# Kernel optimization log

Hardware: AMD Instinct MI355X
Metric: run time of the kernel (lower is better)

The kernel has to match this reference:

```python
import jax, jax.numpy as jnp
import numpy as np

B, D, H, O = 8192, 1024, 4096, 1024
E, S = 8, 2  # routed experts, shared experts


def setup_inputs() -> dict:
    key = jax.random.key(0)
    ks = jax.random.split(key, 12)
    sd = lambda n: 1.0 / np.sqrt(n)
    return {
        "x": jax.random.normal(ks[0], (B, D), jnp.float32),
        "W1": jax.random.normal(ks[1], (E, D, H), jnp.float32) * sd(D),
        "b1": jnp.zeros((E, H), jnp.float32),
        "W2": jax.random.normal(ks[2], (E, H, O), jnp.float32) * sd(H),
        "b2": jnp.zeros((E, O), jnp.float32),
        "Ws1": jax.random.normal(ks[3], (S, D, H), jnp.float32) * sd(D),
        "bs1": jnp.zeros((S, H), jnp.float32),
        "Ws2": jax.random.normal(ks[4], (S, H, O), jnp.float32) * sd(H),
        "bs2": jnp.zeros((S, O), jnp.float32),
        "Wg": jax.random.normal(ks[5], (D, E + S), jnp.float32) * sd(D),
        "bg": jnp.zeros((E + S,), jnp.float32),
        "k": 2,
    }


def _expert_mlp(x, W1, b1, W2, b2):
    # x: [B,D], W1: [n,D,H] -> [B,n,O]; dropout is identity in eval mode
    h = jax.nn.relu(jnp.einsum("bd,ndh->bnh", x, W1) + b1[None])
    return jnp.einsum("bnh,nho->bno", h, W2) + b2[None]


def reference(x, W1, b1, W2, b2, Ws1, bs1, Ws2, bs2, Wg, bg, k):
    gate_scores = jax.nn.softmax(x @ Wg + bg, axis=-1)        # [B, S+E]
    shared_gate = gate_scores[:, :S]                          # [B, S]
    expert_gate = gate_scores[:, S:]                          # [B, E]

    expert_outputs = _expert_mlp(x, W1, b1, W2, b2)           # [B, E, O]
    shared_outputs = _expert_mlp(x, Ws1, bs1, Ws2, bs2)       # [B, S, O]
    shared_output = jnp.einsum("bs,bso->bo", shared_gate, shared_outputs)

    # sparse top-k combine (vectorized equivalent of the per-sample loop)
    topk_score, topk_idx = jax.lax.top_k(expert_gate, k)      # [B, k]
    gathered = jnp.take_along_axis(expert_outputs, topk_idx[:, :, None], axis=1)  # [B,k,O]
    output = jnp.einsum("bk,bko->bo", topk_score, gathered) + shared_output
    return output
```

## Files before the change

kernel.cpp:

```cpp
#include <hip/hip_runtime.h>
#include <stdint.h>

#define Bn 8192
#define Dn 1024
#define Hn 4096
#define On 1024
#define En 8
#define Sn 2

typedef __attribute__((ext_vector_type(8))) short short8;
typedef __attribute__((ext_vector_type(4))) float f32x4;
typedef __attribute__((ext_vector_type(16))) float f32x16;

__device__ __forceinline__ unsigned short f2bf(float f) {
  unsigned int u = __float_as_uint(f);
  u += 0x7fff + ((u >> 16) & 1);
  return (unsigned short)(u >> 16);
}

__device__ __forceinline__ void gload16(const void* g, void* l) {
  __builtin_amdgcn_global_load_lds(
      (const __attribute__((address_space(1))) unsigned int*)g,
      (__attribute__((address_space(3))) unsigned int*)l, 16, 0, 0);
}

__global__ __launch_bounds__(256) void gate_k(
    const float* __restrict__ x, const float* __restrict__ Wg,
    const float* __restrict__ bg, unsigned short* __restrict__ xb,
    float* __restrict__ rw, int* __restrict__ ri) {
  {
    size_t base = (size_t)blockIdx.x * 1024;
    const float4* xi = (const float4*)x + base;
    ushort4* xo = (ushort4*)xb + base;
#pragma unroll
    for (int k2 = 0; k2 < 4; k2++) {
      float4 v = xi[k2 * 256 + threadIdx.x];
      ushort4 o;
      o.x = f2bf(v.x); o.y = f2bf(v.y); o.z = f2bf(v.z); o.w = f2bf(v.w);
      xo[k2 * 256 + threadIdx.x] = o;
    }
  }
  __shared__ __align__(16) float wgs[Dn * 10];
  for (int i = threadIdx.x; i < 2560; i += 256)
    ((float4*)wgs)[i] = ((const float4*)Wg)[i];
  __syncthreads();
  int lane = threadIdx.x & 63, wave = threadIdx.x >> 6;
  int r = blockIdx.x * 4 + wave;
  const float* xr = x + (size_t)r * Dn;
  float p[10];
#pragma unroll
  for (int j = 0; j < 10; j++) p[j] = 0.f;
  for (int d = lane; d < Dn; d += 64) {
    float xv = xr[d];
#pragma unroll
    for (int j = 0; j < 10; j++) p[j] += xv * wgs[d * 10 + j];
  }
#pragma unroll
  for (int off = 32; off; off >>= 1)
#pragma unroll
    for (int j = 0; j < 10; j++) p[j] += __shfl_xor(p[j], off);
  float mx = -1e30f;
#pragma unroll
  for (int j = 0; j < 10; j++) { p[j] += bg[j]; mx = fmaxf(mx, p[j]); }
  float s = 0.f;
#pragma unroll
  for (int j = 0; j < 10; j++) { p[j] = expf(p[j] - mx); s += p[j]; }
  float inv = 1.f / s;
  int i0 = 2, i1 = 2; float v0 = -1e30f, v1 = -1e30f;
#pragma unroll
  for (int j = 2; j < 10; j++) {
    float v = p[j];
    if (v > v0) { v1 = v0; i1 = i0; v0 = v; i0 = j; }
    else if (v > v1) { v1 = v; i1 = j; }
  }
  if (lane == 0) {
    rw[r * 4 + 0] = v0 * inv;
    rw[r * 4 + 1] = v1 * inv;
    rw[r * 4 + 2] = p[0] * inv;
    rw[r * 4 + 3] = p[1] * inv;
    ri[r * 2 + 0] = i0 - 2;
    ri[r * 2 + 1] = i1 - 2;
  }
}

__global__ __launch_bounds__(256) void count_k(const int* __restrict__ ri,
                                               int* __restrict__ cnt) {
  int c[8];
#pragma unroll
  for (int j = 0; j < 8; j++) c[j] = 0;
  int base = blockIdx.x * 1024;
  for (int i = threadIdx.x; i < 1024; i += 256) {
    int e = ri[base + i];
#pragma unroll
    for (int j = 0; j < 8; j++) c[j] += (e == j) ? 1 : 0;
  }
#pragma unroll
  for (int j = 0; j < 8; j++)
#pragma unroll
    for (int off = 32; off; off >>= 1) c[j] += __shfl_xor(c[j], off);
  __shared__ int sc[4][8];
  int wv = threadIdx.x >> 6, lane = threadIdx.x & 63;
  if (lane == 0)
#pragma unroll
    for (int j = 0; j < 8; j++) sc[wv][j] = c[j];
  __syncthreads();
  if (threadIdx.x < 8)
    atomicAdd(&cnt[threadIdx.x], sc[0][threadIdx.x] + sc[1][threadIdx.x] +
                                 sc[2][threadIdx.x] + sc[3][threadIdx.x]);
}

__global__ __launch_bounds__(256) void tcvt_all(
    const float* __restrict__ W1, const float* __restrict__ W2,
    const float* __restrict__ Ws1, const float* __restrict__ Ws2,
    unsigned short* __restrict__ w1t, unsigned short* __restrict__ w2t,
    unsigned short* __restrict__ ws1t, unsigned short* __restrict__ ws2t) {
  __shared__ float t[128][65];
  int bid = blockIdx.x;
  int u = bid >> 9, r = bid & 511;
  const float* in; unsigned short* out; int Kd, Nd;
  if (u < 8)       { Kd = Dn; Nd = Hn; in = W1  + (size_t)u * Dn * Hn;        out = w1t  + (size_t)u * Dn * Hn; }
  else if (u < 16) { Kd = Hn; Nd = On; in = W2  + (size_t)(u - 8) * Hn * On;  out = w2t  + (size_t)(u - 8) * Hn * On; }
  else if (u < 18) { Kd = Dn; Nd = Hn; in = Ws1 + (size_t)(u - 16) * Dn * Hn; out = ws1t + (size_t)(u - 16) * Dn * Hn; }
  else             { Kd = Hn; Nd = On; in = Ws2 + (size_t)(u - 18) * Hn * On; out = ws2t + (size_t)(u - 18) * Hn * On; }
  int by, bx;
  if (Kd == Dn) { by = (r & 7) * 128;  bx = (r >> 3) * 64; }
  else          { by = (r & 31) * 128; bx = (r >> 5) * 64; }
  int tid = threadIdx.x;
#pragma unroll
  for (int q = 0; q < 8; q++) {
    int idx = q * 256 + tid;
    int k = idx >> 4, f4 = (idx & 15) * 4;
    float4 v = *(const float4*)&in[(size_t)(by + k) * Nd + bx + f4];
    t[k][f4] = v.x; t[k][f4 + 1] = v.y; t[k][f4 + 2] = v.z; t[k][f4 + 3] = v.w;
  }
  __syncthreads();
  int KC = Kd >> 3;
#pragma unroll
  for (int p = 0; p < 4; p++) {
    int idx = p * 256 + tid;
    int nl = idx & 63, kgi = idx >> 6;
    int kg = kgi * 8;
    int ng = bx + nl;
    short8 v;
#pragma unroll
    for (int j = 0; j < 8; j++) v[j] = (short)f2bf(t[kg + j][nl]);
    size_t o = ((((size_t)(ng >> 8) * KC + (by >> 3) + kgi) * 256 + (ng & 255)) << 3);
    *(short8*)&out[o] = v;
  }
}

__global__ __launch_bounds__(256) void build_k(
    const float* __restrict__ rw, const int* __restrict__ ri,
    const int* __restrict__ cnt, int* __restrict__ cnt2,
    int* __restrict__ slot_row, float* __restrict__ slot_w,
    int* __restrict__ slot_dst) {
  __shared__ int lcnt[8], lbase[8];
  int tid = threadIdx.x;
  if (tid < 8) lcnt[tid] = 0;
  __syncthreads();
  int r = blockIdx.x * 256 + tid;
  int e0 = ri[r * 2 + 0], e1 = ri[r * 2 + 1];
  int rk0 = atomicAdd(&lcnt[e0], 1);
  int rk1 = atomicAdd(&lcnt[e1], 1);
  __syncthreads();
  if (tid < 8) lbase[tid] = atomicAdd(&cnt2[tid], lcnt[tid]);
  __syncthreads();
  int off0 = 0, off1 = 0;
#pragma unroll
  for (int i = 0; i < 8; i++) {
    int ci = cnt[i];
    off0 += (i < e0) ? ci : 0;
    off1 += (i < e1) ? ci : 0;
  }
  int s0 = off0 + lbase[e0] + rk0;
  int s1 = off1 + lbase[e1] + rk1;
  slot_row[s0] = r; slot_w[s0] = rw[r * 4 + 0]; slot_dst[s0] = r * 4 + 0;
  slot_row[s1] = r; slot_w[s1] = rw[r * 4 + 1]; slot_dst[s1] = r * 4 + 1;
#pragma unroll
  for (int s = 0; s < 2; s++) {
    int slot = 16384 + s * Bn + r;
    slot_row[slot] = r;
    slot_w[slot] = rw[r * 4 + 2 + s];
    slot_dst[slot] = r * 4 + 2 + s;
  }
}


__global__ __launch_bounds__(512, 4) void gemm1_u(
    const unsigned short* __restrict__ xb,
    const unsigned short* __restrict__ w1c, const unsigned short* __restrict__ ws1c,
    const float* __restrict__ b1, const float* __restrict__ bs1,
    const int* __restrict__ cnt, const int* __restrict__ slotRow,
    unsigned short* __restrict__ h, int ubase, int hsh) {
  int total = gridDim.x;
  int gid = blockIdx.x;
  int swz = (gid & 7) * (total >> 3) + (gid >> 3);
  int u = ubase + (swz >> 10);
  int rem = swz & 1023;
  int mt = rem & 63;
  int nt = rem >> 6;

  int M, off, hoff;
  const unsigned short* Bte; const float* be;
  if (u < 8) {
    M = cnt[u]; off = 0;
    for (int i = 0; i < u; i++) off += cnt[i];
    hoff = off;
    Bte = w1c + (size_t)u * Hn * Dn; be = b1 + (size_t)u * Hn;
  } else {
    int s = u - 8;
    M = Bn; off = 16384 + s * Bn; hoff = hsh + s * Bn;
    Bte = ws1c + (size_t)s * Hn * Dn; be = bs1 + (size_t)s * Hn;
  }
  int mbase = mt * 128;
  if (mbase >= M) return;
  int n0 = nt * 256;

  __shared__ __align__(16) unsigned short shb[36864];

  int tid = threadIdx.x;
  int lane = tid & 63, wv = tid >> 6;
  int wm = wv >> 2, wn = wv & 3;
  int l31 = lane & 31, l5 = lane >> 5;
  int rswA = (l31 >> 1) & 3;

  int scol = (((tid & 3) ^ ((tid >> 3) & 3)) * 8);
  int mi = mbase + (tid >> 2);
  if (mi > M - 1) mi = M - 1;
  int grow = slotRow[off + mi];
  const unsigned short* agp = xb + (size_t)grow * Dn + scol;
  const unsigned short* Bnt = Bte + (size_t)nt * 262144;
  const unsigned short* bgp0 = Bnt + (((size_t)(tid >> 8) * 256 + (tid & 255)) << 3);
  const unsigned short* bgp1 = bgp0 + 4096;

  f32x16 acc[2][2];
#pragma unroll
  for (int i = 0; i < 2; i++)
#pragma unroll
    for (int j = 0; j < 2; j++)
#pragma unroll
      for (int q = 0; q < 16; q++) acc[i][j][q] = 0.f;

  auto STAGE = [&](int slot, int tt) {
    int so = slot * 12288;
    gload16(agp + tt * 32, &shb[so + wv * 512]);
    gload16(bgp0 + tt * 8192, &shb[so + 4096 + wv * 512]);
    gload16(bgp1 + tt * 8192, &shb[so + 8192 + wv * 512]);
  };
  auto COMPUTE = [&](int slot) {
    int so = slot * 12288;
#pragma unroll
    for (int kk = 0; kk < 2; kk++) {
      int cA = (((kk * 2 + l5) ^ rswA) * 8);
      short8 a0 = *(const short8*)&shb[so + (wm * 64 + l31) * 32 + cA];
      short8 a1 = *(const short8*)&shb[so + (wm * 64 + 32 + l31) * 32 + cA];
      int cB = (kk * 2 + l5) * 256;
      short8 b0 = *(const short8*)&shb[so + 4096 + (cB + wn * 64 + l31) * 8];
      short8 b1 = *(const short8*)&shb[so + 4096 + (cB + wn * 64 + 32 + l31) * 8];
      acc[0][0] = __builtin_amdgcn_mfma_f32_32x32x16_bf16(a0, b0, acc[0][0], 0, 0, 0);
      acc[0][1] = __builtin_amdgcn_mfma_f32_32x32x16_bf16(a0, b1, acc[0][1], 0, 0, 0);
      acc[1][0] = __builtin_amdgcn_mfma_f32_32x32x16_bf16(a1, b0, acc[1][0], 0, 0, 0);
      acc[1][1] = __builtin_amdgcn_mfma_f32_32x32x16_bf16(a1, b1, acc[1][1], 0, 0, 0);
    }
  };

  const int NT = Dn >> 5;
  int sA = 0, sB = 1, sC = 2;
  STAGE(0, 0);
  STAGE(1, 1);
  for (int t = 0; t < NT; ++t) {
    int tn = (t + 2 < NT) ? (t + 2) : (NT - 1);
    STAGE(sC, tn);
    asm volatile("s_waitcnt vmcnt(6)" ::: "memory");
    asm volatile("s_barrier" ::: "memory");
    COMPUTE(sA);
    asm volatile("s_barrier" ::: "memory");
    int tmp = sA; sA = sB; sB = sC; sC = tmp;
  }

  float bev[2];
#pragma unroll
  for (int g = 0; g < 2; g++) bev[g] = be[n0 + wn * 64 + g * 32 + l31];
#pragma unroll
  for (int i = 0; i < 2; i++) {
#pragma unroll
    for (int reg = 0; reg < 16; reg++) {
      int rr = (reg & 3) + 8 * (reg >> 2) + 4 * l5;
      int m = mbase + wm * 64 + i * 32 + rr;
      if (m < M) {
        size_t hrow = (size_t)(hoff + m) * Hn;
#pragma unroll
        for (int g = 0; g < 2; g++) {
          int n = n0 + wn * 64 + g * 32 + l31;
          float v = acc[i][g][reg] + bev[g];
          h[hrow + n] = f2bf(fmaxf(v, 0.f));
        }
      }
    }
  }
}

__global__ __launch_bounds__(512, 4) void gemm2_u(
    const unsigned short* __restrict__ hin,
    const unsigned short* __restrict__ w2c, const unsigned short* __restrict__ ws2c,
    const float* __restrict__ b2, const float* __restrict__ bs2,
    const int* __restrict__ cnt, const float* __restrict__ slotW,
    const int* __restrict__ slotDst, float* __restrict__ outp, int ubase, int hsh) {
  int total = gridDim.x;
  int gid = blockIdx.x;
  int swz = (gid & 7) * (total >> 3) + (gid >> 3);
  int u = ubase + (swz >> 8);
  int rem = swz & 255;
  int mt = rem & 63;
  int nt = rem >> 6;

  int M, off, hoff;
  const unsigned short* Bte; const float* be;
  if (u < 8) {
    M = cnt[u]; off = 0;
    for (int i = 0; i < u; i++) off += cnt[i];
    hoff = off;
    Bte = w2c + (size_t)u * On * Hn; be = b2 + (size_t)u * On;
  } else {
    int s = u - 8;
    M = Bn; off = 16384 + s * Bn; hoff = hsh + s * Bn;
    Bte = ws2c + (size_t)s * On * Hn; be = bs2 + (size_t)s * On;
  }
  int mbase = mt * 128;
  if (mbase >= M) return;
  int n0 = nt * 256;

  __shared__ __align__(16) unsigned short shb[36864];

  int tid = threadIdx.x;
  int lane = tid & 63, wv = tid >> 6;
  int wm = wv >> 2, wn = wv & 3;
  int l31 = lane & 31, l5 = lane >> 5;
  int rswA = (l31 >> 1) & 3;

  int scol = (((tid & 3) ^ ((tid >> 3) & 3)) * 8);
  int mi = mbase + (tid >> 2);
  if (mi > M - 1) mi = M - 1;
  const unsigned short* agp = hin + (size_t)(hoff + mi) * Hn + scol;
  const unsigned short* Bnt = Bte + (size_t)nt * 1048576;
  const unsigned short* bgp0 = Bnt + (((size_t)(tid >> 8) * 256 + (tid & 255)) << 3);
  const unsigned short* bgp1 = bgp0 + 4096;

  f32x16 acc[2][2];
#pragma unroll
  for (int i = 0; i < 2; i++)
#pragma unroll
    for (int j = 0; j < 2; j++)
#pragma unroll
      for (int q = 0; q < 16; q++) acc[i][j][q] = 0.f;

  auto STAGE = [&](int slot, int tt) {
    int so = slot * 12288;
    gload16(agp + tt * 32, &shb[so + wv * 512]);
    gload16(bgp0 + tt * 8192, &shb[so + 4096 + wv * 512]);
    gload16(bgp1 + tt * 8192, &shb[so + 8192 + wv * 512]);
  };
  auto COMPUTE = [&](int slot) {
    int so = slot * 12288;
#pragma unroll
    for (int kk = 0; kk < 2; kk++) {
      int cA = (((kk * 2 + l5) ^ rswA) * 8);
      short8 a0 = *(const short8*)&shb[so + (wm * 64 + l31) * 32 + cA];
      short8 a1 = *(const short8*)&shb[so + (wm * 64 + 32 + l31) * 32 + cA];
      int cB = (kk * 2 + l5) * 256;
      short8 b0 = *(const short8*)&shb[so + 4096 + (cB + wn * 64 + l31) * 8];
      short8 b1 = *(const short8*)&shb[so + 4096 + (cB + wn * 64 + 32 + l31) * 8];
      acc[0][0] = __builtin_amdgcn_mfma_f32_32x32x16_bf16(a0, b0, acc[0][0], 0, 0, 0);
      acc[0][1] = __builtin_amdgcn_mfma_f32_32x32x16_bf16(a0, b1, acc[0][1], 0, 0, 0);
      acc[1][0] = __builtin_amdgcn_mfma_f32_32x32x16_bf16(a1, b0, acc[1][0], 0, 0, 0);
      acc[1][1] = __builtin_amdgcn_mfma_f32_32x32x16_bf16(a1, b1, acc[1][1], 0, 0, 0);
    }
  };

  const int NT = Hn >> 5;
  int sA = 0, sB = 1, sC = 2;
  STAGE(0, 0);
  STAGE(1, 1);
  for (int t = 0; t < NT; ++t) {
    int tn = (t + 2 < NT) ? (t + 2) : (NT - 1);
    STAGE(sC, tn);
    asm volatile("s_waitcnt vmcnt(6)" ::: "memory");
    asm volatile("s_barrier" ::: "memory");
    COMPUTE(sA);
    asm volatile("s_barrier" ::: "memory");
    int tmp = sA; sA = sB; sB = sC; sC = tmp;
  }

  float bev[2];
#pragma unroll
  for (int g = 0; g < 2; g++) bev[g] = be[n0 + wn * 64 + g * 32 + l31];
#pragma unroll
  for (int i = 0; i < 2; i++) {
#pragma unroll
    for (int reg = 0; reg < 16; reg++) {
      int rr = (reg & 3) + 8 * (reg >> 2) + 4 * l5;
      int m = mbase + wm * 64 + i * 32 + rr;
      if (m < M) {
        float wgt = slotW[off + m];
        size_t orow = (size_t)(slotDst[off + m] >> 2) * On;
#pragma unroll
        for (int g = 0; g < 2; g++) {
          int n = n0 + wn * 64 + g * 32 + l31;
          atomicAdd(&outp[orow + n], wgt * (acc[i][g][reg] + bev[g]));
        }
      }
    }
  }
}

extern "C" void kernel_launch(void* const* d_in, const int* in_sizes, int n_in,
                              void* d_out, int out_size, void* d_ws, size_t ws_size,
                              hipStream_t stream) {
  const float* x   = (const float*)d_in[0];
  const float* W1  = (const float*)d_in[1];
  const float* b1  = (const float*)d_in[2];
  const float* W2  = (const float*)d_in[3];
  const float* b2  = (const float*)d_in[4];
  const float* Ws1 = (const float*)d_in[5];
  const float* bs1 = (const float*)d_in[6];
  const float* Ws2 = (const float*)d_in[7];
  const float* bs2 = (const float*)d_in[8];
  const float* Wg  = (const float*)d_in[9];
  const float* bg  = (const float*)d_in[10];
  float* out = (float*)d_out;

  char* w = (char*)d_ws;
  size_t p = 0;
  auto alloc = [&](size_t n) { char* r = w + p; p = (p + n + 255) & ~(size_t)255; return r; };
  unsigned short* xb   = (unsigned short*)alloc((size_t)Bn * Dn * 2);
  unsigned short* w1t  = (unsigned short*)alloc((size_t)En * Hn * Dn * 2);
  unsigned short* w2t  = (unsigned short*)alloc((size_t)En * On * Hn * 2);
  unsigned short* ws1t = (unsigned short*)alloc((size_t)Sn * Hn * Dn * 2);
  unsigned short* ws2t = (unsigned short*)alloc((size_t)Sn * On * Hn * 2);
  unsigned short* hbuf = (unsigned short*)alloc((size_t)16384 * Hn * 2);
  float* rw            = (float*)alloc((size_t)Bn * 4 * 4);
  int* ri              = (int*)alloc((size_t)Bn * 2 * 4);
  int* ctrl            = (int*)alloc(256);
  int* slot_row        = (int*)alloc((size_t)32768 * 4);
  float* slot_w        = (float*)alloc((size_t)32768 * 4);
  int* slot_dst        = (int*)alloc((size_t)32768 * 4);
  if (p > ws_size) return;

  int* cnt  = ctrl;
  int* cnt2 = ctrl + 8;

  hipMemsetAsync(ctrl, 0, 64, stream);
  hipMemsetAsync(out, 0, (size_t)Bn * On * sizeof(float), stream);
  gate_k<<<2048, 256, 0, stream>>>(x, Wg, bg, xb, rw, ri);
  tcvt_all<<<10240, 256, 0, stream>>>(W1, W2, Ws1, Ws2, w1t, w2t, ws1t, ws2t);
  count_k<<<16, 256, 0, stream>>>(ri, cnt);
  build_k<<<32, 256, 0, stream>>>(rw, ri, cnt, cnt2, slot_row, slot_w, slot_dst);

  gemm1_u<<<8 * 1024, 512, 0, stream>>>(xb, w1t, ws1t, b1, bs1, cnt, slot_row,
                                        hbuf, 0, 0);
  gemm2_u<<<8 * 256, 512, 0, stream>>>(hbuf, w2t, ws2t, b2, bs2, cnt, slot_w,
                                       slot_dst, out, 0, 0);
  gemm1_u<<<2 * 1024, 512, 0, stream>>>(xb, w1t, ws1t, b1, bs1, cnt, slot_row,
                                        hbuf, 8, 0);
  gemm2_u<<<2 * 256, 512, 0, stream>>>(hbuf, w2t, ws2t, b2, bs2, cnt, slot_w,
                                       slot_dst, out, 8, 0);
}
```

Before: 873.7 us.

## Use double-buffered LDS pipeline and replace atomic combine with per-slot buffer reduction

Both GEMM kernels drop from a triple-buffered to a double-buffered LDS pipeline, cutting shared memory per block so more blocks fit per CU (launch bounds raised to 6). The GEMM2 epilogue now writes weighted outputs to a per-(row, slot) buffer Y instead of doing atomicAdd into the output. A new final kernel sums the four slots per row, which also removes the output memset. This trades atomic contention for an extra 128MB write and read pass, and shortens prefetch depth, which may expose load latency.

```diff
diff --git a/kernel.cpp b/kernel.cpp
--- a/kernel.cpp
+++ b/kernel.cpp
@@ -186,7 +186,7 @@
 }
 
 
-__global__ __launch_bounds__(512, 4) void gemm1_u(
+__global__ __launch_bounds__(512, 6) void gemm1_u(
     const unsigned short* __restrict__ xb,
     const unsigned short* __restrict__ w1c, const unsigned short* __restrict__ ws1c,
     const float* __restrict__ b1, const float* __restrict__ bs1,
@@ -216,7 +216,7 @@
   if (mbase >= M) return;
   int n0 = nt * 256;
 
-  __shared__ __align__(16) unsigned short shb[36864];
+  __shared__ __align__(16) unsigned short shb[24576];
 
   int tid = threadIdx.x;
   int lane = tid & 63, wv = tid >> 6;
@@ -265,17 +265,16 @@
   };
 
   const int NT = Dn >> 5;
-  int sA = 0, sB = 1, sC = 2;
   STAGE(0, 0);
-  STAGE(1, 1);
+  int cur = 0;
   for (int t = 0; t < NT; ++t) {
-    int tn = (t + 2 < NT) ? (t + 2) : (NT - 1);
-    STAGE(sC, tn);
-    asm volatile("s_waitcnt vmcnt(6)" ::: "memory");
+    int tn = (t + 1 < NT) ? (t + 1) : (NT - 1);
+    STAGE(cur ^ 1, tn);
+    asm volatile("s_waitcnt vmcnt(3)" ::: "memory");
     asm volatile("s_barrier" ::: "memory");
-    COMPUTE(sA);
+    COMPUTE(cur);
     asm volatile("s_barrier" ::: "memory");
-    int tmp = sA; sA = sB; sB = sC; sC = tmp;
+    cur ^= 1;
   }
 
   float bev[2];
@@ -300,12 +299,12 @@
   }
 }
 
-__global__ __launch_bounds__(512, 4) void gemm2_u(
+__global__ __launch_bounds__(512, 6) void gemm2_u(
     const unsigned short* __restrict__ hin,
     const unsigned short* __restrict__ w2c, const unsigned short* __restrict__ ws2c,
     const float* __restrict__ b2, const float* __restrict__ bs2,
     const int* __restrict__ cnt, const float* __restrict__ slotW,
-    const int* __restrict__ slotDst, float* __restrict__ outp, int ubase, int hsh) {
+    const int* __restrict__ slotDst, float* __restrict__ Y, int ubase, int hsh) {
   int total = gridDim.x;
   int gid = blockIdx.x;
   int swz = (gid & 7) * (total >> 3) + (gid >> 3);
@@ -330,7 +329,7 @@
   if (mbase >= M) return;
   int n0 = nt * 256;
 
-  __shared__ __align__(16) unsigned short shb[36864];
+  __shared__ __align__(16) unsigned short shb[24576];
 
   int tid = threadIdx.x;
   int lane = tid & 63, wv = tid >> 6;
@@ -378,17 +377,16 @@
   };
 
   const int NT = Hn >> 5;
-  int sA = 0, sB = 1, sC = 2;
   STAGE(0, 0);
-  STAGE(1, 1);
+  int cur = 0;
   for (int t = 0; t < NT; ++t) {
-    int tn = (t + 2 < NT) ? (t + 2) : (NT - 1);
-    STAGE(sC, tn);
-    asm volatile("s_waitcnt vmcnt(6)" ::: "memory");
+    int tn = (t + 1 < NT) ? (t + 1) : (NT - 1);
+    STAGE(cur ^ 1, tn);
+    asm volatile("s_waitcnt vmcnt(3)" ::: "memory");
     asm volatile("s_barrier" ::: "memory");
-    COMPUTE(sA);
+    COMPUTE(cur);
     asm volatile("s_barrier" ::: "memory");
-    int tmp = sA; sA = sB; sB = sC; sC = tmp;
+    cur ^= 1;
   }
 
   float bev[2];
@@ -402,15 +400,32 @@
       int m = mbase + wm * 64 + i * 32 + rr;
       if (m < M) {
         float wgt = slotW[off + m];
-        size_t orow = (size_t)(slotDst[off + m] >> 2) * On;
+        size_t yrow = (size_t)slotDst[off + m] * On;
 #pragma unroll
         for (int g = 0; g < 2; g++) {
           int n = n0 + wn * 64 + g * 32 + l31;
-          atomicAdd(&outp[orow + n], wgt * (acc[i][g][reg] + bev[g]));
+          Y[yrow + n] = wgt * (acc[i][g][reg] + bev[g]);
         }
       }
     }
   }
+}
+
+__global__ void final_k(const float* __restrict__ Y, float* __restrict__ out) {
+  int i = blockIdx.x * 256 + threadIdx.x;
+  int b = i >> 8;
+  int c = i & 255;
+  const float4* y = (const float4*)Y;
+  float4 a0 = y[((size_t)b * 4 + 0) * 256 + c];
+  float4 a1 = y[((size_t)b * 4 + 1) * 256 + c];
+  float4 a2 = y[((size_t)b * 4 + 2) * 256 + c];
+  float4 a3 = y[((size_t)b * 4 + 3) * 256 + c];
+  float4 o;
+  o.x = a0.x + a1.x + a2.x + a3.x;
+  o.y = a0.y + a1.y + a2.y + a3.y;
+  o.z = a0.z + a1.z + a2.z + a3.z;
+  o.w = a0.w + a1.w + a2.w + a3.w;
+  ((float4*)out)[i] = o;
 }
 
 extern "C" void kernel_launch(void* const* d_in, const int* in_sizes, int n_in,
@@ -438,6 +453,7 @@
   unsigned short* ws1t = (unsigned short*)alloc((size_t)Sn * Hn * Dn * 2);
   unsigned short* ws2t = (unsigned short*)alloc((size_t)Sn * On * Hn * 2);
   unsigned short* hbuf = (unsigned short*)alloc((size_t)16384 * Hn * 2);
+  float* Y             = (float*)alloc((size_t)Bn * 4 * On * 4);
   float* rw            = (float*)alloc((size_t)Bn * 4 * 4);
   int* ri              = (int*)alloc((size_t)Bn * 2 * 4);
   int* ctrl            = (int*)alloc(256);
@@ -450,7 +466,6 @@
   int* cnt2 = ctrl + 8;
 
   hipMemsetAsync(ctrl, 0, 64, stream);
-  hipMemsetAsync(out, 0, (size_t)Bn * On * sizeof(float), stream);
   gate_k<<<2048, 256, 0, stream>>>(x, Wg, bg, xb, rw, ri);
   tcvt_all<<<10240, 256, 0, stream>>>(W1, W2, Ws1, Ws2, w1t, w2t, ws1t, ws2t);
   count_k<<<16, 256, 0, stream>>>(ri, cnt);
@@ -459,9 +474,10 @@
   gemm1_u<<<8 * 1024, 512, 0, stream>>>(xb, w1t, ws1t, b1, bs1, cnt, slot_row,
                                         hbuf, 0, 0);
   gemm2_u<<<8 * 256, 512, 0, stream>>>(hbuf, w2t, ws2t, b2, bs2, cnt, slot_w,
-                                       slot_dst, out, 0, 0);
+                                       slot_dst, Y, 0, 0);
   gemm1_u<<<2 * 1024, 512, 0, stream>>>(xb, w1t, ws1t, b1, bs1, cnt, slot_row,
                                         hbuf, 8, 0);
   gemm2_u<<<2 * 256, 512, 0, stream>>>(hbuf, w2t, ws2t, b2, bs2, cnt, slot_w,
-                                       slot_dst, out, 8, 0);
-}
+                                       slot_dst, Y, 8, 0);
+  final_k<<<8192, 256, 0, stream>>>(Y, out);
+}
```

Result: slower. 1.458 ms (+66.9%).

## Replace atomic output accumulation with staged buffer and fused shared-expert combine

Applied to the files above, without the earlier changes.

Routed-expert GEMM2 now writes weighted results non-atomically into a per-(row,k) staging buffer Y instead of atomically adding into the output. A new shared-expert GEMM2 kernel computes both shared experts per tile, applies gate weights, adds the two routed contributions from Y, and writes the final output directly, which removes the output memset and all float atomics. It adds a 64MB intermediate buffer write/read and a serial two-phase K loop per block with smaller N tiles.

```diff
diff --git a/kernel.cpp b/kernel.cpp
--- a/kernel.cpp
+++ b/kernel.cpp
@@ -174,14 +174,14 @@
   }
   int s0 = off0 + lbase[e0] + rk0;
   int s1 = off1 + lbase[e1] + rk1;
-  slot_row[s0] = r; slot_w[s0] = rw[r * 4 + 0]; slot_dst[s0] = r * 4 + 0;
-  slot_row[s1] = r; slot_w[s1] = rw[r * 4 + 1]; slot_dst[s1] = r * 4 + 1;
+  slot_row[s0] = r; slot_w[s0] = rw[r * 4 + 0]; slot_dst[s0] = r * 2 + 0;
+  slot_row[s1] = r; slot_w[s1] = rw[r * 4 + 1]; slot_dst[s1] = r * 2 + 1;
 #pragma unroll
   for (int s = 0; s < 2; s++) {
     int slot = 16384 + s * Bn + r;
     slot_row[slot] = r;
     slot_w[slot] = rw[r * 4 + 2 + s];
-    slot_dst[slot] = r * 4 + 2 + s;
+    slot_dst[slot] = 0;
   }
 }
 
@@ -302,30 +302,24 @@
 
 __global__ __launch_bounds__(512, 4) void gemm2_u(
     const unsigned short* __restrict__ hin,
-    const unsigned short* __restrict__ w2c, const unsigned short* __restrict__ ws2c,
-    const float* __restrict__ b2, const float* __restrict__ bs2,
+    const unsigned short* __restrict__ w2c,
+    const float* __restrict__ b2,
     const int* __restrict__ cnt, const float* __restrict__ slotW,
-    const int* __restrict__ slotDst, float* __restrict__ outp, int ubase, int hsh) {
+    const int* __restrict__ slotDst, float* __restrict__ Y) {
   int total = gridDim.x;
   int gid = blockIdx.x;
   int swz = (gid & 7) * (total >> 3) + (gid >> 3);
-  int u = ubase + (swz >> 8);
+  int u = swz >> 8;
   int rem = swz & 255;
   int mt = rem & 63;
   int nt = rem >> 6;
 
-  int M, off, hoff;
-  const unsigned short* Bte; const float* be;
-  if (u < 8) {
-    M = cnt[u]; off = 0;
-    for (int i = 0; i < u; i++) off += cnt[i];
-    hoff = off;
-    Bte = w2c + (size_t)u * On * Hn; be = b2 + (size_t)u * On;
-  } else {
-    int s = u - 8;
-    M = Bn; off = 16384 + s * Bn; hoff = hsh + s * Bn;
-    Bte = ws2c + (size_t)s * On * Hn; be = bs2 + (size_t)s * On;
-  }
+  int M = cnt[u], off = 0;
+  for (int i = 0; i < u; i++) off += cnt[i];
+  int hoff = off;
+  const unsigned short* Bte = w2c + (size_t)u * On * Hn;
+  const float* be = b2 + (size_t)u * On;
+
   int mbase = mt * 128;
   if (mbase >= M) return;
   int n0 = nt * 256;
@@ -402,13 +396,112 @@
       int m = mbase + wm * 64 + i * 32 + rr;
       if (m < M) {
         float wgt = slotW[off + m];
-        size_t orow = (size_t)(slotDst[off + m] >> 2) * On;
+        size_t yrow = (size_t)slotDst[off + m] * On;
 #pragma unroll
         for (int g = 0; g < 2; g++) {
           int n = n0 + wn * 64 + g * 32 + l31;
-          atomicAdd(&outp[orow + n], wgt * (acc[i][g][reg] + bev[g]));
+          Y[yrow + n] = wgt * (acc[i][g][reg] + bev[g]);
         }
       }
+    }
+  }
+}
+
+__global__ __launch_bounds__(512, 4) void gemm2s_m(
+    const unsigned short* __restrict__ hin,
+    const unsigned short* __restrict__ ws2c,
+    const float* __restrict__ bs2, const float* __restrict__ rw,
+    const float* __restrict__ Y, float* __restrict__ outp) {
+  int total = gridDim.x;
+  int gid = blockIdx.x;
+  int swz = (gid & 7) * (total >> 3) + (gid >> 3);
+  int mt = swz & 63;
+  int nt = swz >> 6;
+  int mbase = mt * 128;
+  int n0 = nt * 128;
+
+  __shared__ __align__(16) unsigned short shb[24576];
+
+  int tid = threadIdx.x;
+  int lane = tid & 63, wv = tid >> 6;
+  int wm = wv >> 2, wn = wv & 3;
+  int l31 = lane & 31, l5 = lane >> 5;
+  int rswA = (l31 >> 1) & 3;
+
+  int scol = (((tid & 3) ^ ((tid >> 3) & 3)) * 8);
+  const unsigned short* agp0 = hin + (size_t)(mbase + (tid >> 2)) * Hn + scol;
+  const unsigned short* agp1 = agp0 + (size_t)8192 * Hn;
+  size_t bcol = (((size_t)(tid >> 7) * 256 + (nt & 1) * 128 + (tid & 127)) << 3);
+  const unsigned short* bgp0 = ws2c + (size_t)(nt >> 1) * 1048576 + bcol;
+  const unsigned short* bgp1 = bgp0 + (size_t)Hn * On;
+
+  f32x16 acc0[2], acc1[2];
+#pragma unroll
+  for (int i = 0; i < 2; i++)
+#pragma unroll
+    for (int q = 0; q < 16; q++) { acc0[i][q] = 0.f; acc1[i][q] = 0.f; }
+
+  auto STAGE = [&](int slot, int tt, const unsigned short* ag, const unsigned short* bg) {
+    int so = slot * 8192;
+    gload16(ag + tt * 32, &shb[so + wv * 512]);
+    gload16(bg + (size_t)tt * 8192, &shb[so + 4096 + wv * 512]);
+  };
+  auto COMPUTE = [&](int slot, f32x16 (&ac)[2]) {
+    int so = slot * 8192;
+#pragma unroll
+    for (int kk = 0; kk < 2; kk++) {
+      int cA = (((kk * 2 + l5) ^ rswA) * 8);
+      short8 a0 = *(const short8*)&shb[so + (wm * 64 + l31) * 32 + cA];
+      short8 a1 = *(const short8*)&shb[so + (wm * 64 + 32 + l31) * 32 + cA];
+      int cB = (kk * 2 + l5) * 128;
+      short8 b0 = *(const short8*)&shb[so + 4096 + (cB + wn * 32 + l31) * 8];
+      ac[0] = __builtin_amdgcn_mfma_f32_32x32x16_bf16(a0, b0, ac[0], 0, 0, 0);
+      ac[1] = __builtin_amdgcn_mfma_f32_32x32x16_bf16(a1, b0, ac[1], 0, 0, 0);
+    }
+  };
+
+  {
+    int sA = 0, sB = 1, sC = 2;
+    STAGE(0, 0, agp0, bgp0);
+    STAGE(1, 1, agp0, bgp0);
+    for (int t = 0; t < 128; ++t) {
+      int tn = (t + 2 < 128) ? (t + 2) : 127;
+      STAGE(sC, tn, agp0, bgp0);
+      asm volatile("s_waitcnt vmcnt(4)" ::: "memory");
+      asm volatile("s_barrier" ::: "memory");
+      COMPUTE(sA, acc0);
+      asm volatile("s_barrier" ::: "memory");
+      int tmp = sA; sA = sB; sB = sC; sC = tmp;
+    }
+  }
+  {
+    int sA = 0, sB = 1, sC = 2;
+    STAGE(0, 0, agp1, bgp1);
+    STAGE(1, 1, agp1, bgp1);
+    for (int t = 0; t < 128; ++t) {
+      int tn = (t + 2 < 128) ? (t + 2) : 127;
+      STAGE(sC, tn, agp1, bgp1);
+      asm volatile("s_waitcnt vmcnt(4)" ::: "memory");
+      asm volatile("s_barrier" ::: "memory");
+      COMPUTE(sA, acc1);
+      asm volatile("s_barrier" ::: "memory");
+      int tmp = sA; sA = sB; sB = sC; sC = tmp;
+    }
+  }
+
+  int n = n0 + wn * 32 + l31;
+  float be0 = bs2[n];
+  float be1 = bs2[On + n];
+#pragma unroll
+  for (int i = 0; i < 2; i++) {
+#pragma unroll
+    for (int reg = 0; reg < 16; reg++) {
+      int rr = (reg & 3) + 8 * (reg >> 2) + 4 * l5;
+      int m = mbase + wm * 64 + i * 32 + rr;
+      float w0 = rw[m * 4 + 2], w1 = rw[m * 4 + 3];
+      float v = w0 * (acc0[i][reg] + be0) + w1 * (acc1[i][reg] + be1)
+              + Y[((size_t)m * 2 + 0) * On + n] + Y[((size_t)m * 2 + 1) * On + n];
+      outp[(size_t)m * On + n] = v;
     }
   }
 }
@@ -438,6 +531,7 @@
   unsigned short* ws1t = (unsigned short*)alloc((size_t)Sn * Hn * Dn * 2);
   unsigned short* ws2t = (unsigned short*)alloc((size_t)Sn * On * Hn * 2);
   unsigned short* hbuf = (unsigned short*)alloc((size_t)16384 * Hn * 2);
+  float* Y             = (float*)alloc((size_t)Bn * 2 * On * 4);
   float* rw            = (float*)alloc((size_t)Bn * 4 * 4);
   int* ri              = (int*)alloc((size_t)Bn * 2 * 4);
   int* ctrl            = (int*)alloc(256);
@@ -450,7 +544,6 @@
   int* cnt2 = ctrl + 8;
 
   hipMemsetAsync(ctrl, 0, 64, stream);
-  hipMemsetAsync(out, 0, (size_t)Bn * On * sizeof(float), stream);
   gate_k<<<2048, 256, 0, stream>>>(x, Wg, bg, xb, rw, ri);
   tcvt_all<<<10240, 256, 0, stream>>>(W1, W2, Ws1, Ws2, w1t, w2t, ws1t, ws2t);
   count_k<<<16, 256, 0, stream>>>(ri, cnt);
@@ -458,10 +551,8 @@
 
   gemm1_u<<<8 * 1024, 512, 0, stream>>>(xb, w1t, ws1t, b1, bs1, cnt, slot_row,
                                         hbuf, 0, 0);
-  gemm2_u<<<8 * 256, 512, 0, stream>>>(hbuf, w2t, ws2t, b2, bs2, cnt, slot_w,
-                                       slot_dst, out, 0, 0);
+  gemm2_u<<<8 * 256, 512, 0, stream>>>(hbuf, w2t, b2, cnt, slot_w, slot_dst, Y);
   gemm1_u<<<2 * 1024, 512, 0, stream>>>(xb, w1t, ws1t, b1, bs1, cnt, slot_row,
                                         hbuf, 8, 0);
-  gemm2_u<<<2 * 256, 512, 0, stream>>>(hbuf, w2t, ws2t, b2, bs2, cnt, slot_w,
-                                       slot_dst, out, 8, 0);
-}
+  gemm2s_m<<<512, 512, 0, stream>>>(hbuf, ws2t, bs2, rw, Y, out);
+}
```

After: 859.6 us. About the same (-1.6%).

## Replace atomic output accumulation with per-slot buffer and final reduction kernel

Applied to the files above, without the earlier changes.

gemm2 now writes each weighted expert contribution into a dedicated slot of a [B,4,O] buffer instead of issuing float atomicAdds into the output, and a new final_k kernel sums the four slots per row. This also removes the output memset. The bf16 conversion of x is folded into the gate kernel's existing row loop, and the weight transpose kernel now reads global memory directly instead of staging through an LDS tile. The goal is to cut atomic contention and memset traffic, at the cost of an extra 128MB write plus read. The uncoalesced strided reads in the transpose kernel may cost more than the LDS staging they replace.

```diff
diff --git a/kernel.cpp b/kernel.cpp
--- a/kernel.cpp
+++ b/kernel.cpp
@@ -28,18 +28,6 @@
     const float* __restrict__ x, const float* __restrict__ Wg,
     const float* __restrict__ bg, unsigned short* __restrict__ xb,
     float* __restrict__ rw, int* __restrict__ ri) {
-  {
-    size_t base = (size_t)blockIdx.x * 1024;
-    const float4* xi = (const float4*)x + base;
-    ushort4* xo = (ushort4*)xb + base;
-#pragma unroll
-    for (int k2 = 0; k2 < 4; k2++) {
-      float4 v = xi[k2 * 256 + threadIdx.x];
-      ushort4 o;
-      o.x = f2bf(v.x); o.y = f2bf(v.y); o.z = f2bf(v.z); o.w = f2bf(v.w);
-      xo[k2 * 256 + threadIdx.x] = o;
-    }
-  }
   __shared__ __align__(16) float wgs[Dn * 10];
   for (int i = threadIdx.x; i < 2560; i += 256)
     ((float4*)wgs)[i] = ((const float4*)Wg)[i];
@@ -47,11 +35,13 @@
   int lane = threadIdx.x & 63, wave = threadIdx.x >> 6;
   int r = blockIdx.x * 4 + wave;
   const float* xr = x + (size_t)r * Dn;
+  unsigned short* xbr = xb + (size_t)r * Dn;
   float p[10];
 #pragma unroll
   for (int j = 0; j < 10; j++) p[j] = 0.f;
   for (int d = lane; d < Dn; d += 64) {
     float xv = xr[d];
+    xbr[d] = f2bf(xv);
 #pragma unroll
     for (int j = 0; j < 10; j++) p[j] += xv * wgs[d * 10 + j];
   }
@@ -114,7 +104,6 @@
     const float* __restrict__ Ws1, const float* __restrict__ Ws2,
     unsigned short* __restrict__ w1t, unsigned short* __restrict__ w2t,
     unsigned short* __restrict__ ws1t, unsigned short* __restrict__ ws2t) {
-  __shared__ float t[128][65];
   int bid = blockIdx.x;
   int u = bid >> 9, r = bid & 511;
   const float* in; unsigned short* out; int Kd, Nd;
@@ -126,24 +115,18 @@
   if (Kd == Dn) { by = (r & 7) * 128;  bx = (r >> 3) * 64; }
   else          { by = (r & 31) * 128; bx = (r >> 5) * 64; }
   int tid = threadIdx.x;
-#pragma unroll
-  for (int q = 0; q < 8; q++) {
-    int idx = q * 256 + tid;
-    int k = idx >> 4, f4 = (idx & 15) * 4;
-    float4 v = *(const float4*)&in[(size_t)(by + k) * Nd + bx + f4];
-    t[k][f4] = v.x; t[k][f4 + 1] = v.y; t[k][f4 + 2] = v.z; t[k][f4 + 3] = v.w;
-  }
-  __syncthreads();
+  int nl = tid & 63;
+  int kq = tid >> 6;
   int KC = Kd >> 3;
+  int ng = bx + nl;
 #pragma unroll
   for (int p = 0; p < 4; p++) {
-    int idx = p * 256 + tid;
-    int nl = idx & 63, kgi = idx >> 6;
+    int kgi = p * 4 + kq;
     int kg = kgi * 8;
-    int ng = bx + nl;
     short8 v;
 #pragma unroll
-    for (int j = 0; j < 8; j++) v[j] = (short)f2bf(t[kg + j][nl]);
+    for (int j = 0; j < 8; j++)
+      v[j] = (short)f2bf(in[(size_t)(by + kg + j) * Nd + ng]);
     size_t o = ((((size_t)(ng >> 8) * KC + (by >> 3) + kgi) * 256 + (ng & 255)) << 3);
     *(short8*)&out[o] = v;
   }
@@ -305,7 +288,7 @@
     const unsigned short* __restrict__ w2c, const unsigned short* __restrict__ ws2c,
     const float* __restrict__ b2, const float* __restrict__ bs2,
     const int* __restrict__ cnt, const float* __restrict__ slotW,
-    const int* __restrict__ slotDst, float* __restrict__ outp, int ubase, int hsh) {
+    const int* __restrict__ slotDst, float* __restrict__ Y, int ubase, int hsh) {
   int total = gridDim.x;
   int gid = blockIdx.x;
   int swz = (gid & 7) * (total >> 3) + (gid >> 3);
@@ -402,15 +385,32 @@
       int m = mbase + wm * 64 + i * 32 + rr;
       if (m < M) {
         float wgt = slotW[off + m];
-        size_t orow = (size_t)(slotDst[off + m] >> 2) * On;
+        size_t yrow = (size_t)slotDst[off + m] * On;
 #pragma unroll
         for (int g = 0; g < 2; g++) {
           int n = n0 + wn * 64 + g * 32 + l31;
-          atomicAdd(&outp[orow + n], wgt * (acc[i][g][reg] + bev[g]));
+          Y[yrow + n] = wgt * (acc[i][g][reg] + bev[g]);
         }
       }
     }
   }
+}
+
+__global__ void final_k(const float* __restrict__ Y, float* __restrict__ out) {
+  int i = blockIdx.x * 256 + threadIdx.x;
+  int b = i >> 8;
+  int c = i & 255;
+  const float4* y = (const float4*)Y;
+  float4 a0 = y[((size_t)b * 4 + 0) * 256 + c];
+  float4 a1 = y[((size_t)b * 4 + 1) * 256 + c];
+  float4 a2 = y[((size_t)b * 4 + 2) * 256 + c];
+  float4 a3 = y[((size_t)b * 4 + 3) * 256 + c];
+  float4 o;
+  o.x = a0.x + a1.x + a2.x + a3.x;
+  o.y = a0.y + a1.y + a2.y + a3.y;
+  o.z = a0.z + a1.z + a2.z + a3.z;
+  o.w = a0.w + a1.w + a2.w + a3.w;
+  ((float4*)out)[i] = o;
 }
 
 extern "C" void kernel_launch(void* const* d_in, const int* in_sizes, int n_in,
@@ -438,6 +438,7 @@
   unsigned short* ws1t = (unsigned short*)alloc((size_t)Sn * Hn * Dn * 2);
   unsigned short* ws2t = (unsigned short*)alloc((size_t)Sn * On * Hn * 2);
   unsigned short* hbuf = (unsigned short*)alloc((size_t)16384 * Hn * 2);
+  float* Y             = (float*)alloc((size_t)Bn * 4 * On * 4);
   float* rw            = (float*)alloc((size_t)Bn * 4 * 4);
   int* ri              = (int*)alloc((size_t)Bn * 2 * 4);
   int* ctrl            = (int*)alloc(256);
@@ -450,7 +451,6 @@
   int* cnt2 = ctrl + 8;
 
   hipMemsetAsync(ctrl, 0, 64, stream);
-  hipMemsetAsync(out, 0, (size_t)Bn * On * sizeof(float), stream);
   gate_k<<<2048, 256, 0, stream>>>(x, Wg, bg, xb, rw, ri);
   tcvt_all<<<10240, 256, 0, stream>>>(W1, W2, Ws1, Ws2, w1t, w2t, ws1t, ws2t);
   count_k<<<16, 256, 0, stream>>>(ri, cnt);
@@ -459,9 +459,10 @@
   gemm1_u<<<8 * 1024, 512, 0, stream>>>(xb, w1t, ws1t, b1, bs1, cnt, slot_row,
                                         hbuf, 0, 0);
   gemm2_u<<<8 * 256, 512, 0, stream>>>(hbuf, w2t, ws2t, b2, bs2, cnt, slot_w,
-                                       slot_dst, out, 0, 0);
+                                       slot_dst, Y, 0, 0);
   gemm1_u<<<2 * 1024, 512, 0, stream>>>(xb, w1t, ws1t, b1, bs1, cnt, slot_row,
                                         hbuf, 8, 0);
   gemm2_u<<<2 * 256, 512, 0, stream>>>(hbuf, w2t, ws2t, b2, bs2, cnt, slot_w,
-                                       slot_dst, out, 8, 0);
-}
+                                       slot_dst, Y, 8, 0);
+  final_k<<<8192, 256, 0, stream>>>(Y, out);
+}
```

Result: faster. 855.6 us (-2.1%).
